# Kernel optimization log

Hardware: AMD Instinct MI355X
Metric: run time of the kernel (lower is better)

Reference implementation:

```python
import jax, jax.numpy as jnp
import numpy as np

N_NODES = 100000
N_EDGES = 1600000
IN_C, HID_C, OUT_C = 128, 128, 64


def gcn_conv(x, src, dst, ew, W, b, n_nodes):
    """PyG GCNConv: symmetric-normalized aggregation with added self-loops.

    out = D^{-1/2} (A + I) D^{-1/2} (x @ W) + b,  D = deg(A+I)
    """
    h = x @ W  # [N, C_out]
    # degree at target nodes, including self-loop weight of 1
    deg = jax.ops.segment_sum(ew, dst, num_segments=n_nodes) + 1.0  # [N]
    dinv = jnp.where(deg > 0, jax.lax.rsqrt(deg), 0.0)
    norm = dinv[src] * ew * dinv[dst]  # [E]
    # gather-scale-scatter over edges + self-loop term (norm_ii = 1/deg_i)
    agg = jax.ops.segment_sum(h[src] * norm[:, None], dst, num_segments=n_nodes)
    agg = agg + h * (dinv * dinv)[:, None]
    return agg + b


def setup_inputs() -> dict:
    key = jax.random.key(0)
    ks = jax.random.split(key, 7)
    x = jax.random.normal(ks[0], (N_NODES, IN_C), dtype=jnp.float32)
    edge_index = jax.random.randint(ks[1], (2, N_EDGES), 0, N_NODES, dtype=jnp.int32)
    edge_weight = jax.random.uniform(ks[2], (N_EDGES,), dtype=jnp.float32)
    W1 = jax.random.normal(ks[3], (IN_C, HID_C), dtype=jnp.float32) / np.sqrt(IN_C)
    b1 = jnp.zeros((HID_C,), dtype=jnp.float32)
    W2 = jax.random.normal(ks[4], (HID_C, OUT_C), dtype=jnp.float32) / np.sqrt(HID_C)
    b2 = jnp.zeros((OUT_C,), dtype=jnp.float32)
    return {"x": x, "edge_index": edge_index, "edge_weight": edge_weight,
            "W1": W1, "b1": b1, "W2": W2, "b2": b2}


def reference(x, edge_index, edge_weight, W1, b1, W2, b2):
    src, dst = edge_index[0], edge_index[1]
    n = x.shape[0]
    h = gcn_conv(x, src, dst, edge_weight, W1, b1, n)
    h = jax.nn.relu(h)
    out = gcn_conv(h, src, dst, edge_weight, W2, b2, n)
    return out
```

## Files before the change

kernel.cpp:

```cpp
#include <hip/hip_runtime.h>


#define N_NODES 100000
#define CHUNK   2048
#define NBUCK   196
#define BSHIFT  9
#define BNODES  512
#define CAP     10240

typedef __attribute__((ext_vector_type(8))) short bf16x8;
typedef __attribute__((ext_vector_type(4))) float f32x4;

__device__ __forceinline__ unsigned bf16r(float f) {
    unsigned u = __float_as_uint(f);
    return (u + 0x7fffu + ((u >> 16) & 1u)) >> 16;
}
__device__ __forceinline__ float bf_lo(unsigned u) { return __uint_as_float(u << 16); }
__device__ __forceinline__ float bf_hi(unsigned u) { return __uint_as_float(u & 0xffff0000u); }

__device__ __forceinline__ void fma8(float* a, uint4 u, float w) {
    a[0] = fmaf(bf_lo(u.x), w, a[0]); a[1] = fmaf(bf_hi(u.x), w, a[1]);
    a[2] = fmaf(bf_lo(u.y), w, a[2]); a[3] = fmaf(bf_hi(u.y), w, a[3]);
    a[4] = fmaf(bf_lo(u.z), w, a[4]); a[5] = fmaf(bf_hi(u.z), w, a[5]);
    a[6] = fmaf(bf_lo(u.w), w, a[6]); a[7] = fmaf(bf_hi(u.w), w, a[7]);
}


__global__ __launch_bounds__(256) void prepA1_kernel(
    const int* __restrict__ dst, const float* __restrict__ W1,
    const float* __restrict__ W2, unsigned* __restrict__ Wt1,
    unsigned* __restrict__ Wt2, int* __restrict__ histmat, int E)
{
    __shared__ int hist[256];
    int t = threadIdx.x;
    if (blockIdx.x == 0) {
        for (int f = t; f < 128 * 64; f += 256) {
            int c = f % 128, j = f / 128;
            Wt1[c * 64 + j] = bf16r(W1[(size_t)(2 * j) * 128 + c]) |
                              (bf16r(W1[(size_t)(2 * j + 1) * 128 + c]) << 16);
        }
        return;
    }
    if (blockIdx.x == 1) {
        for (int f = t; f < 64 * 64; f += 256) {
            int c = f % 64, j = f / 64;
            Wt2[c * 64 + j] = bf16r(W2[(size_t)(2 * j) * 64 + c]) |
                              (bf16r(W2[(size_t)(2 * j + 1) * 64 + c]) << 16);
        }
        return;
    }
    int blk = blockIdx.x - 2;
    hist[t] = 0;
    __syncthreads();
    int e0 = blk * CHUNK;
    int nv = min(CHUNK, E - e0);
#pragma unroll
    for (int j = 0; j < CHUNK / 256; ++j) {
        int idx = t + j * 256;
        if (idx < nv) atomicAdd(&hist[dst[e0 + idx] >> BSHIFT], 1);
    }
    __syncthreads();
    histmat[blk * 256 + t] = hist[t];
}


__global__ __launch_bounds__(256) void scanB_kernel(
    int* __restrict__ histmat, int* __restrict__ bucketSize, int NBLK)
{
    __shared__ int sums[256];
    int b = blockIdx.x, t = threadIdx.x;
    const int PER = (NBLK + 255) / 256;
    int loc[8];
    int s = 0;
#pragma unroll 8
    for (int j = 0; j < PER; ++j) {
        int r = t * PER + j;
        int v = (r < NBLK) ? histmat[r * 256 + b] : 0;
        loc[j] = v; s += v;
    }
    sums[t] = s;
    __syncthreads();
    int v = s;
#pragma unroll
    for (int off = 1; off < 256; off <<= 1) {
        int a = (t >= off) ? sums[t - off] : 0;
        __syncthreads();
        sums[t] += a;
        __syncthreads();
    }
    if (t == 255) bucketSize[b] = sums[255];
    int run = sums[t] - v;
#pragma unroll 8
    for (int j = 0; j < PER; ++j) {
        int r = t * PER + j;
        if (r < NBLK) { histmat[r * 256 + b] = run; run += loc[j]; }
    }
}


__global__ __launch_bounds__(256) void a2_kernel(
    const int* __restrict__ src, const int* __restrict__ dst,
    const float* __restrict__ ew, const int* __restrict__ histmat,
    uint2* __restrict__ csrTmp, int E)
{
    __shared__ int hist[256], sc[256], exc[256], lcur[256], basel[256];
    __shared__ uint2 ent[CHUNK];
    __shared__ unsigned short bof[CHUNK];

    int t = threadIdx.x, blk = blockIdx.x;
    hist[t] = 0; lcur[t] = 0;
    basel[t] = histmat[blk * 256 + t];
    __syncthreads();

    int e0 = blk * CHUNK;
    int nv = min(CHUNK, E - e0);
    int dv[CHUNK / 256]; int sv[CHUNK / 256]; unsigned wv[CHUNK / 256];
#pragma unroll
    for (int j = 0; j < CHUNK / 256; ++j) {
        int idx = t + j * 256;
        if (idx < nv) {
            int e = e0 + idx;
            dv[j] = dst[e]; sv[j] = src[e]; wv[j] = __float_as_uint(ew[e]);
            atomicAdd(&hist[dv[j] >> BSHIFT], 1);
        } else dv[j] = -1;
    }
    __syncthreads();
    int hv = hist[t];
    sc[t] = hv;
    __syncthreads();
#pragma unroll
    for (int off = 1; off < 256; off <<= 1) {
        int a = (t >= off) ? sc[t - off] : 0;
        __syncthreads();
        sc[t] += a;
        __syncthreads();
    }
    exc[t] = sc[t] - hv;
    __syncthreads();
#pragma unroll
    for (int j = 0; j < CHUNK / 256; ++j) {
        if (dv[j] >= 0) {
            int b  = dv[j] >> BSHIFT;
            int dl = dv[j] & (BNODES - 1);
            int p  = exc[b] + atomicAdd(&lcur[b], 1);
            ent[p] = make_uint2(((unsigned)dl << 17) | (unsigned)sv[j], wv[j]);
            bof[p] = (unsigned short)b;
        }
    }
    __syncthreads();
#pragma unroll
    for (int j = 0; j < CHUNK / 256; ++j) {
        int i = t + j * 256;
        if (i < nv) {
            int b = bof[i];
            csrTmp[(size_t)b * CAP + basel[b] + (i - exc[b])] = ent[i];
        }
    }
}


__global__ __launch_bounds__(1024) void bucketB_kernel(
    const uint2* __restrict__ csrTmp, const int* __restrict__ bucketSize,
    float* __restrict__ dinv, uint2* __restrict__ nodeinfo,
    uint2* __restrict__ csrF, int N)
{
    __shared__ uint2 ent[CAP];
    __shared__ unsigned long long dc[BNODES];
    __shared__ int scn[BNODES], beg[BNODES], cur[BNODES];
    int b = blockIdx.x, t = threadIdx.x;
    if (t < BNODES) { dc[t] = 0ull; cur[t] = 0; }
    __syncthreads();

    int sz = min(bucketSize[b], CAP);
    const uint2* reg = csrTmp + (size_t)b * CAP;
    for (int i = t; i < sz; i += 1024) {
        uint2 en = reg[i];
        ent[i] = en;
        int dl = (int)(en.x >> 17);
        unsigned fx = (unsigned)__float2uint_rn(__uint_as_float(en.y) * 16777216.0f);
        atomicAdd(&dc[dl], (1ull << 32) | (unsigned long long)fx);
    }
    __syncthreads();

    int cnt = 0; float dv = 1.0f;
    if (t < BNODES) {
        unsigned long long v = dc[t];
        cnt = (int)(v >> 32);
        dv = rsqrtf((float)(unsigned)(v & 0xffffffffull) * (1.0f / 16777216.0f) + 1.0f);
        scn[t] = cnt;
    }
    __syncthreads();
#pragma unroll
    for (int off = 1; off < BNODES; off <<= 1) {
        int a = 0;
        if (t < BNODES && t >= off) a = scn[t - off];
        __syncthreads();
        if (t < BNODES) scn[t] += a;
        __syncthreads();
    }
    if (t < BNODES) {
        int excl = scn[t] - cnt;
        beg[t] = excl;
        int gn = b * BNODES + t;
        if (gn < N) {
            dinv[gn] = dv;
            nodeinfo[gn] = make_uint2((unsigned)(b * CAP + excl), (unsigned)cnt);
        }
    }
    __syncthreads();

    uint2* outreg = csrF + (size_t)b * CAP;
    for (int i = t; i < sz; i += 1024) {
        uint2 en = ent[i];
        int dl = (int)(en.x >> 17);
        int p  = beg[dl] + atomicAdd(&cur[dl], 1);
        outreg[p] = make_uint2(en.x & 0x1FFFFu, en.y);
    }
}


__global__ __launch_bounds__(256) void gemm1_kernel(
    const float* __restrict__ Xf, const unsigned* __restrict__ Wt,
    const float* __restrict__ dinv, unsigned* __restrict__ Hb, int M)
{
    constexpr int LW = 68, KU = 64;
    __shared__ unsigned sA[64 * LW];
    __shared__ unsigned sB[128 * LW];
    __shared__ float sD[64];
    const int t = threadIdx.x;
    const int rbase = blockIdx.x * 64;

    if (t < 64) sD[t] = (rbase + t < M) ? dinv[rbase + t] : 0.f;
    for (int f = t; f < 128 * 16; f += 256) {
        int c = f >> 4, qd = f & 15;
        *(uint4*)&sB[c * LW + qd * 4] = *(const uint4*)&Wt[c * KU + qd * 4];
    }
    for (int f = t; f < 64 * 32; f += 256) {
        int r = f >> 5, c4 = f & 31;
        int gr = rbase + r;
        float4 v = make_float4(0.f, 0.f, 0.f, 0.f);
        if (gr < M) v = *(const float4*)&Xf[(size_t)gr * 128 + c4 * 4];
        sA[r * LW + c4 * 2]     = bf16r(v.x) | (bf16r(v.y) << 16);
        sA[r * LW + c4 * 2 + 1] = bf16r(v.z) | (bf16r(v.w) << 16);
    }
    __syncthreads();

    const int wave = t >> 6, lane = t & 63;
    const int quad = lane >> 4, lr = lane & 15;
    const int n0 = wave * 32;

    f32x4 acc[4][2];
#pragma unroll
    for (int mi = 0; mi < 4; ++mi)
#pragma unroll
        for (int ni = 0; ni < 2; ++ni)
            acc[mi][ni] = (f32x4){0.f, 0.f, 0.f, 0.f};

#pragma unroll
    for (int ks = 0; ks < 4; ++ks) {
        int ko = ks * 16 + quad * 4;
        bf16x8 b0 = *(const bf16x8*)&sB[(n0 + lr) * LW + ko];
        bf16x8 b1 = *(const bf16x8*)&sB[(n0 + 16 + lr) * LW + ko];
#pragma unroll
        for (int mi = 0; mi < 4; ++mi) {
            bf16x8 a = *(const bf16x8*)&sA[(mi * 16 + lr) * LW + ko];
            acc[mi][0] = __builtin_amdgcn_mfma_f32_16x16x32_bf16(a, b0, acc[mi][0], 0, 0, 0);
            acc[mi][1] = __builtin_amdgcn_mfma_f32_16x16x32_bf16(a, b1, acc[mi][1], 0, 0, 0);
        }
    }
    __syncthreads();

    unsigned short* sO = (unsigned short*)sA;
#pragma unroll
    for (int mi = 0; mi < 4; ++mi)
#pragma unroll
        for (int ni = 0; ni < 2; ++ni)
#pragma unroll
            for (int r = 0; r < 4; ++r) {
                int row = mi * 16 + quad * 4 + r;
                sO[row * (2 * LW) + n0 + ni * 16 + lr] =
                    (unsigned short)bf16r(acc[mi][ni][r] * sD[row]);
            }
    __syncthreads();

    for (int f = t; f < 64 * 64; f += 256) {
        int row = f >> 6, cu = f & 63;
        int gr = rbase + row;
        if (gr < M) Hb[(size_t)gr * 64 + cu] = sA[row * LW + cu];
    }
}


__global__ __launch_bounds__(512, 4) void gg_kernel(
    const uint2* __restrict__ nodeinfo, const uint2* __restrict__ csr,
    const uint4* __restrict__ Hb4,
    const float* __restrict__ dinv, const float* __restrict__ bias,
    const unsigned* __restrict__ Wt2, unsigned* __restrict__ H2, int N)
{
    __shared__ __align__(16) unsigned sG[16 * 68];
    __shared__ __align__(16) float    sO[16 * 68];
    __shared__ float sDi[16];

    const int t = threadIdx.x, wave = t >> 6, lane = t & 63;
    const int q = lane >> 4, cg = lane & 15;
    const int nb = blockIdx.x * 16;
    if (t < 16) sDi[t] = dinv[nb + t];

    const int m0 = wave * 2, m1 = m0 + 1;
    const int n0 = nb + m0, n1 = nb + m1;

    float one0 = (q == 0) ? 1.f : 0.f;
    float acc0[8], acc1[8];
    {
        uint4 su = Hb4[(size_t)n0 * 16 + cg];
        uint4 sv = Hb4[(size_t)n1 * 16 + cg];
        acc0[0] = bf_lo(su.x) * one0; acc0[1] = bf_hi(su.x) * one0;
        acc0[2] = bf_lo(su.y) * one0; acc0[3] = bf_hi(su.y) * one0;
        acc0[4] = bf_lo(su.z) * one0; acc0[5] = bf_hi(su.z) * one0;
        acc0[6] = bf_lo(su.w) * one0; acc0[7] = bf_hi(su.w) * one0;
        acc1[0] = bf_lo(sv.x) * one0; acc1[1] = bf_hi(sv.x) * one0;
        acc1[2] = bf_lo(sv.y) * one0; acc1[3] = bf_hi(sv.y) * one0;
        acc1[4] = bf_lo(sv.z) * one0; acc1[5] = bf_hi(sv.z) * one0;
        acc1[6] = bf_lo(sv.w) * one0; acc1[7] = bf_hi(sv.w) * one0;
    }
    uint2 i0 = nodeinfo[n0], i1 = nodeinfo[n1];
    int j0 = (int)i0.x, e0v = j0 + (int)i0.y;
    int j1 = (int)i1.x, e1v = j1 + (int)i1.y;

    while (j0 < e0v || j1 < e1v) {
        int cs0 = 0, cs1 = 0; float cw0 = 0.f, cw1 = 0.f;
        if (j0 + lane < e0v) { uint2 p = csr[j0 + lane]; cs0 = (int)p.x; cw0 = __uint_as_float(p.y); }
        if (j1 + lane < e1v) { uint2 p = csr[j1 + lane]; cs1 = (int)p.x; cw1 = __uint_as_float(p.y); }
        int r0 = e0v - j0; int mm0 = r0 < 0 ? 0 : (r0 > 64 ? 64 : r0);
        int r1 = e1v - j1; int mm1 = r1 < 0 ? 0 : (r1 > 64 ? 64 : r1);
        int mmx = mm0 > mm1 ? mm0 : mm1;

        int   s0 = __shfl(cs0, q),  s1 = __shfl(cs1, q);
        float w0 = __shfl(cw0, q),  w1 = __shfl(cw1, q);
        uint4 u0 = Hb4[(size_t)s0 * 16 + cg];
        uint4 u1 = Hb4[(size_t)s1 * 16 + cg];

        for (int k = 0; k < mmx; k += 4) {
            uint4 u0n = u0, u1n = u1;
            float w0n = 0.f, w1n = 0.f;
            if (k + 4 < mmx) {
                int s0n = __shfl(cs0, k + 4 + q), s1n = __shfl(cs1, k + 4 + q);
                w0n = __shfl(cw0, k + 4 + q);     w1n = __shfl(cw1, k + 4 + q);
                u0n = Hb4[(size_t)s0n * 16 + cg];
                u1n = Hb4[(size_t)s1n * 16 + cg];
            }
            fma8(acc0, u0, w0);
            fma8(acc1, u1, w1);
            u0 = u0n; u1 = u1n; w0 = w0n; w1 = w1n;
        }
        j0 += 64; j1 += 64;
    }

#pragma unroll
    for (int v = 0; v < 8; ++v) {
        acc0[v] += __shfl_xor(acc0[v], 16);
        acc0[v] += __shfl_xor(acc0[v], 32);
        acc1[v] += __shfl_xor(acc1[v], 16);
        acc1[v] += __shfl_xor(acc1[v], 32);
    }
    if (q == 0) {
        int c = cg * 8;
        float di0 = dinv[n0];
        uint4 pk;
        pk.x = bf16r(fmaxf(acc0[0] * di0 + bias[c + 0], 0.f)) |
               (bf16r(fmaxf(acc0[1] * di0 + bias[c + 1], 0.f)) << 16);
        pk.y = bf16r(fmaxf(acc0[2] * di0 + bias[c + 2], 0.f)) |
               (bf16r(fmaxf(acc0[3] * di0 + bias[c + 3], 0.f)) << 16);
        pk.z = bf16r(fmaxf(acc0[4] * di0 + bias[c + 4], 0.f)) |
               (bf16r(fmaxf(acc0[5] * di0 + bias[c + 5], 0.f)) << 16);
        pk.w = bf16r(fmaxf(acc0[6] * di0 + bias[c + 6], 0.f)) |
               (bf16r(fmaxf(acc0[7] * di0 + bias[c + 7], 0.f)) << 16);
        *(uint4*)&sG[m0 * 68 + cg * 4] = pk;
        float di1 = dinv[n1];
        pk.x = bf16r(fmaxf(acc1[0] * di1 + bias[c + 0], 0.f)) |
               (bf16r(fmaxf(acc1[1] * di1 + bias[c + 1], 0.f)) << 16);
        pk.y = bf16r(fmaxf(acc1[2] * di1 + bias[c + 2], 0.f)) |
               (bf16r(fmaxf(acc1[3] * di1 + bias[c + 3], 0.f)) << 16);
        pk.z = bf16r(fmaxf(acc1[4] * di1 + bias[c + 4], 0.f)) |
               (bf16r(fmaxf(acc1[5] * di1 + bias[c + 5], 0.f)) << 16);
        pk.w = bf16r(fmaxf(acc1[6] * di1 + bias[c + 6], 0.f)) |
               (bf16r(fmaxf(acc1[7] * di1 + bias[c + 7], 0.f)) << 16);
        *(uint4*)&sG[m1 * 68 + cg * 4] = pk;
    }
    __syncthreads();

    if (wave < 4) {
        const int quad = lane >> 4, lr = lane & 15;
        const int nt0 = wave * 16;
        f32x4 accv = (f32x4){0.f, 0.f, 0.f, 0.f};
#pragma unroll
        for (int ks = 0; ks < 4; ++ks) {
            int ko = ks * 16 + quad * 4;
            bf16x8 av = *(const bf16x8*)&sG[lr * 68 + ko];
            bf16x8 bv = *(const bf16x8*)&Wt2[(nt0 + lr) * 64 + ko];
            accv = __builtin_amdgcn_mfma_f32_16x16x32_bf16(av, bv, accv, 0, 0, 0);
        }
#pragma unroll
        for (int r = 0; r < 4; ++r)
            sO[(quad * 4 + r) * 68 + nt0 + lr] = accv[r];
    }
    __syncthreads();

    if (t < 512) {
        int row = t >> 5, cu = t & 31;
        float sc = sDi[row];
        unsigned pk = bf16r(sO[row * 68 + 2 * cu] * sc) |
                      (bf16r(sO[row * 68 + 2 * cu + 1] * sc) << 16);
        H2[(size_t)(nb + row) * 32 + cu] = pk;
    }
}


__global__ __launch_bounds__(256, 4) void gather64_kernel(
    const uint2* __restrict__ nodeinfo, const uint2* __restrict__ csr,
    const uint4* __restrict__ Hb4,
    const float* __restrict__ dinv, const float* __restrict__ bias,
    float* __restrict__ OUT, int N)
{
    const int wave = threadIdx.x >> 6, lane = threadIdx.x & 63;
    const int n0 = blockIdx.x * 8 + wave * 2, n1 = n0 + 1;
    if (n0 >= N) return;
    const int q  = lane >> 3;
    const int cg = lane & 7;

    float one0 = (q == 0) ? 1.f : 0.f;
    float acc0[8], acc1[8];
    {
        uint4 su = Hb4[(size_t)n0 * 8 + cg];
        uint4 sv = Hb4[(size_t)n1 * 8 + cg];
        acc0[0] = bf_lo(su.x) * one0; acc0[1] = bf_hi(su.x) * one0;
        acc0[2] = bf_lo(su.y) * one0; acc0[3] = bf_hi(su.y) * one0;
        acc0[4] = bf_lo(su.z) * one0; acc0[5] = bf_hi(su.z) * one0;
        acc0[6] = bf_lo(su.w) * one0; acc0[7] = bf_hi(su.w) * one0;
        acc1[0] = bf_lo(sv.x) * one0; acc1[1] = bf_hi(sv.x) * one0;
        acc1[2] = bf_lo(sv.y) * one0; acc1[3] = bf_hi(sv.y) * one0;
        acc1[4] = bf_lo(sv.z) * one0; acc1[5] = bf_hi(sv.z) * one0;
        acc1[6] = bf_lo(sv.w) * one0; acc1[7] = bf_hi(sv.w) * one0;
    }

    uint2 i0 = nodeinfo[n0], i1 = nodeinfo[n1];
    int j0 = (int)i0.x, e0v = j0 + (int)i0.y;
    int j1 = (int)i1.x, e1v = j1 + (int)i1.y;

    while (j0 < e0v || j1 < e1v) {
        int cs0 = 0, cs1 = 0; float cw0 = 0.f, cw1 = 0.f;
        if (j0 + lane < e0v) { uint2 p = csr[j0 + lane]; cs0 = (int)p.x; cw0 = __uint_as_float(p.y); }
        if (j1 + lane < e1v) { uint2 p = csr[j1 + lane]; cs1 = (int)p.x; cw1 = __uint_as_float(p.y); }
        int r0 = e0v - j0; int mm0 = r0 < 0 ? 0 : (r0 > 64 ? 64 : r0);
        int r1 = e1v - j1; int mm1 = r1 < 0 ? 0 : (r1 > 64 ? 64 : r1);
        int mmx = mm0 > mm1 ? mm0 : mm1;

        int   s0 = __shfl(cs0, q),  s1 = __shfl(cs1, q);
        float w0 = __shfl(cw0, q),  w1 = __shfl(cw1, q);
        uint4 u0 = Hb4[(size_t)s0 * 8 + cg];
        uint4 u1 = Hb4[(size_t)s1 * 8 + cg];

        for (int k = 0; k < mmx; k += 8) {
            uint4 u0n = u0, u1n = u1;
            float w0n = 0.f, w1n = 0.f;
            if (k + 8 < mmx) {
                int s0n = __shfl(cs0, k + 8 + q), s1n = __shfl(cs1, k + 8 + q);
                w0n = __shfl(cw0, k + 8 + q);     w1n = __shfl(cw1, k + 8 + q);
                u0n = Hb4[(size_t)s0n * 8 + cg];
                u1n = Hb4[(size_t)s1n * 8 + cg];
            }
            fma8(acc0, u0, w0);
            fma8(acc1, u1, w1);
            u0 = u0n; u1 = u1n; w0 = w0n; w1 = w1n;
        }
        j0 += 64; j1 += 64;
    }

#pragma unroll
    for (int v = 0; v < 8; ++v) {
        acc0[v] += __shfl_xor(acc0[v], 8);
        acc0[v] += __shfl_xor(acc0[v], 16);
        acc0[v] += __shfl_xor(acc0[v], 32);
        acc1[v] += __shfl_xor(acc1[v], 8);
        acc1[v] += __shfl_xor(acc1[v], 16);
        acc1[v] += __shfl_xor(acc1[v], 32);
    }

    int c = cg * 8 + q;
    OUT[(size_t)n0 * 64 + c] = acc0[q] * dinv[n0] + bias[c];
    OUT[(size_t)n1 * 64 + c] = acc1[q] * dinv[n1] + bias[c];
}

static inline size_t align_up(size_t x) { return (x + 255) & ~size_t(255); }

extern "C" void kernel_launch(void* const* d_in, const int* in_sizes, int n_in,
                              void* d_out, int out_size, void* d_ws, size_t ws_size,
                              hipStream_t stream)
{
    const float* x  = (const float*)d_in[0];
    const int*   ei = (const int*)d_in[1];
    const float* ew = (const float*)d_in[2];
    const float* W1 = (const float*)d_in[3];
    const float* b1 = (const float*)d_in[4];
    const float* W2 = (const float*)d_in[5];
    const float* b2 = (const float*)d_in[6];
    float* out = (float*)d_out;

    const int N = N_NODES;
    const int E = in_sizes[2];
    const int* src = ei;
    const int* dst = ei + E;

    const int NBLK = (E + CHUNK - 1) / CHUNK;
    const size_t REGION = (size_t)NBUCK * CAP;

    char* ws = (char*)d_ws;
    int*   histmat   = (int*)ws;   ws += align_up((size_t)NBLK * 256 * 4);
    int*   bucketSize= (int*)ws;   ws += align_up((size_t)NBUCK * 4);
    float* dinv      = (float*)ws; ws += align_up((size_t)N * 4);
    uint2* nodeinfo  = (uint2*)ws; ws += align_up((size_t)N * 8);
    uint2* csrTmp    = (uint2*)ws; ws += align_up(REGION * 8);
    uint2* csrF      = (uint2*)ws; ws += align_up(REGION * 8);
    unsigned* Wt1    = (unsigned*)ws; ws += align_up((size_t)128 * 64 * 4);
    unsigned* Wt2    = (unsigned*)ws; ws += align_up((size_t)64 * 64 * 4);
    unsigned* h1     = (unsigned*)ws; ws += align_up((size_t)N * 64 * 4);
    unsigned* h2     = (unsigned*)ws; ws += align_up((size_t)N * 32 * 4);

    prepA1_kernel<<<NBLK + 2, 256, 0, stream>>>(dst, W1, W2, Wt1, Wt2, histmat, E);
    scanB_kernel<<<NBUCK, 256, 0, stream>>>(histmat, bucketSize, NBLK);
    a2_kernel<<<NBLK, 256, 0, stream>>>(src, dst, ew, histmat, csrTmp, E);
    bucketB_kernel<<<NBUCK, 1024, 0, stream>>>(csrTmp, bucketSize, dinv, nodeinfo, csrF, N);
    gemm1_kernel<<<(N + 63) / 64, 256, 0, stream>>>(x, Wt1, dinv, h1, N);
    gg_kernel<<<N / 16, 512, 0, stream>>>(nodeinfo, csrF, (const uint4*)h1,
                                          dinv, b1, Wt2, h2, N);
    gather64_kernel<<<(N + 7) / 8, 256, 0, stream>>>(
        nodeinfo, csrF, (const uint4*)h2, dinv, b2, out, N);
}
```

Measured before the change: 272.6 us.

## Replace two-pass bucketed CSR build with global atomic count-then-scatter

Replaces the histogram/scan/bucket-partition/local-sort pipeline with a simpler build. Per-node 64-bit atomics on global memory accumulate degree count and fixed-point weight sum. A per-bucket scan then computes node offsets, and a scatter kernel places each edge with a global atomic cursor. This removes the csrTmp intermediate pass and two kernels, at the cost of many contended global atomics and random uncoalesced writes. Edge order within a node becomes nondeterministic.

Result: slower. 387.2 us (+42.0%).

```diff
diff --git a/kernel.cpp b/kernel.cpp
--- a/kernel.cpp
+++ b/kernel.cpp
@@ -2,7 +2,6 @@
 
 
 #define N_NODES 100000
-#define CHUNK   2048
 #define NBUCK   196
 #define BSHIFT  9
 #define BNODES  512
@@ -26,12 +25,12 @@
 }
 
 
-__global__ __launch_bounds__(256) void prepA1_kernel(
-    const int* __restrict__ dst, const float* __restrict__ W1,
-    const float* __restrict__ W2, unsigned* __restrict__ Wt1,
-    unsigned* __restrict__ Wt2, int* __restrict__ histmat, int E)
-{
-    __shared__ int hist[256];
+__global__ __launch_bounds__(256) void prepcnt_kernel(
+    const int* __restrict__ dst, const float* __restrict__ ew,
+    const float* __restrict__ W1, const float* __restrict__ W2,
+    unsigned* __restrict__ Wt1, unsigned* __restrict__ Wt2,
+    unsigned long long* __restrict__ degfx, int E)
+{
     int t = threadIdx.x;
     if (blockIdx.x == 0) {
         for (int f = t; f < 128 * 64; f += 256) {
@@ -49,172 +48,62 @@
         }
         return;
     }
-    int blk = blockIdx.x - 2;
-    hist[t] = 0;
-    __syncthreads();
-    int e0 = blk * CHUNK;
-    int nv = min(CHUNK, E - e0);
-#pragma unroll
-    for (int j = 0; j < CHUNK / 256; ++j) {
-        int idx = t + j * 256;
-        if (idx < nv) atomicAdd(&hist[dst[e0 + idx] >> BSHIFT], 1);
-    }
-    __syncthreads();
-    histmat[blk * 256 + t] = hist[t];
-}
-
-
-__global__ __launch_bounds__(256) void scanB_kernel(
-    int* __restrict__ histmat, int* __restrict__ bucketSize, int NBLK)
-{
-    __shared__ int sums[256];
+    int e0 = (blockIdx.x - 2) * 2048;
+#pragma unroll
+    for (int j = 0; j < 8; ++j) {
+        int idx = e0 + t + j * 256;
+        if (idx < E) {
+            unsigned fx = (unsigned)__float2uint_rn(ew[idx] * 16777216.0f);
+            atomicAdd(&degfx[dst[idx]], (1ull << 32) | (unsigned long long)fx);
+        }
+    }
+}
+
+
+__global__ __launch_bounds__(512) void scanN_kernel(
+    const unsigned long long* __restrict__ degfx, float* __restrict__ dinv,
+    uint2* __restrict__ nodeinfo, int* __restrict__ cur, int N)
+{
+    __shared__ int scn[BNODES];
     int b = blockIdx.x, t = threadIdx.x;
-    const int PER = (NBLK + 255) / 256;
-    int loc[8];
-    int s = 0;
-#pragma unroll 8
-    for (int j = 0; j < PER; ++j) {
-        int r = t * PER + j;
-        int v = (r < NBLK) ? histmat[r * 256 + b] : 0;
-        loc[j] = v; s += v;
-    }
-    sums[t] = s;
-    __syncthreads();
-    int v = s;
-#pragma unroll
-    for (int off = 1; off < 256; off <<= 1) {
-        int a = (t >= off) ? sums[t - off] : 0;
+    int gn = b * BNODES + t;
+    unsigned long long v = (gn < N) ? degfx[gn] : 0ull;
+    int cnt = (int)(v >> 32);
+    float dv = rsqrtf((float)(unsigned)(v & 0xffffffffull) * (1.0f / 16777216.0f) + 1.0f);
+    scn[t] = cnt;
+    __syncthreads();
+#pragma unroll
+    for (int off = 1; off < BNODES; off <<= 1) {
+        int a = (t >= off) ? scn[t - off] : 0;
         __syncthreads();
-        sums[t] += a;
+        scn[t] += a;
         __syncthreads();
     }
-    if (t == 255) bucketSize[b] = sums[255];
-    int run = sums[t] - v;
-#pragma unroll 8
-    for (int j = 0; j < PER; ++j) {
-        int r = t * PER + j;
-        if (r < NBLK) { histmat[r * 256 + b] = run; run += loc[j]; }
-    }
-}
-
-
-__global__ __launch_bounds__(256) void a2_kernel(
+    int excl = scn[t] - cnt;
+    if (gn < N) {
+        dinv[gn] = dv;
+        nodeinfo[gn] = make_uint2((unsigned)(b * CAP + excl), (unsigned)cnt);
+        cur[gn] = 0;
+    }
+}
+
+
+__global__ __launch_bounds__(256) void scatter_kernel(
     const int* __restrict__ src, const int* __restrict__ dst,
-    const float* __restrict__ ew, const int* __restrict__ histmat,
-    uint2* __restrict__ csrTmp, int E)
-{
-    __shared__ int hist[256], sc[256], exc[256], lcur[256], basel[256];
-    __shared__ uint2 ent[CHUNK];
-    __shared__ unsigned short bof[CHUNK];
-
-    int t = threadIdx.x, blk = blockIdx.x;
-    hist[t] = 0; lcur[t] = 0;
-    basel[t] = histmat[blk * 256 + t];
-    __syncthreads();
-
-    int e0 = blk * CHUNK;
-    int nv = min(CHUNK, E - e0);
-    int dv[CHUNK / 256]; int sv[CHUNK / 256]; unsigned wv[CHUNK / 256];
-#pragma unroll
-    for (int j = 0; j < CHUNK / 256; ++j) {
-        int idx = t + j * 256;
-        if (idx < nv) {
-            int e = e0 + idx;
-            dv[j] = dst[e]; sv[j] = src[e]; wv[j] = __float_as_uint(ew[e]);
-            atomicAdd(&hist[dv[j] >> BSHIFT], 1);
-        } else dv[j] = -1;
-    }
-    __syncthreads();
-    int hv = hist[t];
-    sc[t] = hv;
-    __syncthreads();
-#pragma unroll
-    for (int off = 1; off < 256; off <<= 1) {
-        int a = (t >= off) ? sc[t - off] : 0;
-        __syncthreads();
-        sc[t] += a;
-        __syncthreads();
-    }
-    exc[t] = sc[t] - hv;
-    __syncthreads();
-#pragma unroll
-    for (int j = 0; j < CHUNK / 256; ++j) {
-        if (dv[j] >= 0) {
-            int b  = dv[j] >> BSHIFT;
-            int dl = dv[j] & (BNODES - 1);
-            int p  = exc[b] + atomicAdd(&lcur[b], 1);
-            ent[p] = make_uint2(((unsigned)dl << 17) | (unsigned)sv[j], wv[j]);
-            bof[p] = (unsigned short)b;
-        }
-    }
-    __syncthreads();
-#pragma unroll
-    for (int j = 0; j < CHUNK / 256; ++j) {
-        int i = t + j * 256;
-        if (i < nv) {
-            int b = bof[i];
-            csrTmp[(size_t)b * CAP + basel[b] + (i - exc[b])] = ent[i];
-        }
-    }
-}
-
-
-__global__ __launch_bounds__(1024) void bucketB_kernel(
-    const uint2* __restrict__ csrTmp, const int* __restrict__ bucketSize,
-    float* __restrict__ dinv, uint2* __restrict__ nodeinfo,
-    uint2* __restrict__ csrF, int N)
-{
-    __shared__ uint2 ent[CAP];
-    __shared__ unsigned long long dc[BNODES];
-    __shared__ int scn[BNODES], beg[BNODES], cur[BNODES];
-    int b = blockIdx.x, t = threadIdx.x;
-    if (t < BNODES) { dc[t] = 0ull; cur[t] = 0; }
-    __syncthreads();
-
-    int sz = min(bucketSize[b], CAP);
-    const uint2* reg = csrTmp + (size_t)b * CAP;
-    for (int i = t; i < sz; i += 1024) {
-        uint2 en = reg[i];
-        ent[i] = en;
-        int dl = (int)(en.x >> 17);
-        unsigned fx = (unsigned)__float2uint_rn(__uint_as_float(en.y) * 16777216.0f);
-        atomicAdd(&dc[dl], (1ull << 32) | (unsigned long long)fx);
-    }
-    __syncthreads();
-
-    int cnt = 0; float dv = 1.0f;
-    if (t < BNODES) {
-        unsigned long long v = dc[t];
-        cnt = (int)(v >> 32);
-        dv = rsqrtf((float)(unsigned)(v & 0xffffffffull) * (1.0f / 16777216.0f) + 1.0f);
-        scn[t] = cnt;
-    }
-    __syncthreads();
-#pragma unroll
-    for (int off = 1; off < BNODES; off <<= 1) {
-        int a = 0;
-        if (t < BNODES && t >= off) a = scn[t - off];
-        __syncthreads();
-        if (t < BNODES) scn[t] += a;
-        __syncthreads();
-    }
-    if (t < BNODES) {
-        int excl = scn[t] - cnt;
-        beg[t] = excl;
-        int gn = b * BNODES + t;
-        if (gn < N) {
-            dinv[gn] = dv;
-            nodeinfo[gn] = make_uint2((unsigned)(b * CAP + excl), (unsigned)cnt);
-        }
-    }
-    __syncthreads();
-
-    uint2* outreg = csrF + (size_t)b * CAP;
-    for (int i = t; i < sz; i += 1024) {
-        uint2 en = ent[i];
-        int dl = (int)(en.x >> 17);
-        int p  = beg[dl] + atomicAdd(&cur[dl], 1);
-        outreg[p] = make_uint2(en.x & 0x1FFFFu, en.y);
+    const float* __restrict__ ew, const unsigned* __restrict__ nodebase,
+    int* __restrict__ cur, uint2* __restrict__ csrF, int E)
+{
+    int e0 = blockIdx.x * 2048;
+    int t = threadIdx.x;
+#pragma unroll
+    for (int j = 0; j < 8; ++j) {
+        int idx = e0 + t + j * 256;
+        if (idx < E) {
+            int d = dst[idx];
+            unsigned base = nodebase[(size_t)d * 2];
+            int p = atomicAdd(&cur[d], 1);
+            csrF[base + p] = make_uint2((unsigned)src[idx], __float_as_uint(ew[idx]));
+        }
     }
 }
 
@@ -511,26 +400,26 @@
     const int* src = ei;
     const int* dst = ei + E;
 
-    const int NBLK = (E + CHUNK - 1) / CHUNK;
     const size_t REGION = (size_t)NBUCK * CAP;
+    const int EBLK = (E + 2047) / 2048;
 
     char* ws = (char*)d_ws;
-    int*   histmat   = (int*)ws;   ws += align_up((size_t)NBLK * 256 * 4);
-    int*   bucketSize= (int*)ws;   ws += align_up((size_t)NBUCK * 4);
+    unsigned long long* degfx = (unsigned long long*)ws; ws += align_up((size_t)N * 8);
+    int*   cur       = (int*)ws;   ws += align_up((size_t)N * 4);
     float* dinv      = (float*)ws; ws += align_up((size_t)N * 4);
     uint2* nodeinfo  = (uint2*)ws; ws += align_up((size_t)N * 8);
-    uint2* csrTmp    = (uint2*)ws; ws += align_up(REGION * 8);
     uint2* csrF      = (uint2*)ws; ws += align_up(REGION * 8);
     unsigned* Wt1    = (unsigned*)ws; ws += align_up((size_t)128 * 64 * 4);
     unsigned* Wt2    = (unsigned*)ws; ws += align_up((size_t)64 * 64 * 4);
     unsigned* h1     = (unsigned*)ws; ws += align_up((size_t)N * 64 * 4);
     unsigned* h2     = (unsigned*)ws; ws += align_up((size_t)N * 32 * 4);
 
-    prepA1_kernel<<<NBLK + 2, 256, 0, stream>>>(dst, W1, W2, Wt1, Wt2, histmat, E);
-    scanB_kernel<<<NBUCK, 256, 0, stream>>>(histmat, bucketSize, NBLK);
-    a2_kernel<<<NBLK, 256, 0, stream>>>(src, dst, ew, histmat, csrTmp, E);
-    bucketB_kernel<<<NBUCK, 1024, 0, stream>>>(csrTmp, bucketSize, dinv, nodeinfo, csrF, N);
+    hipMemsetAsync(degfx, 0, (size_t)N * 8, stream);
+    prepcnt_kernel<<<EBLK + 2, 256, 0, stream>>>(dst, ew, W1, W2, Wt1, Wt2, degfx, E);
+    scanN_kernel<<<NBUCK, 512, 0, stream>>>(degfx, dinv, nodeinfo, cur, N);
     gemm1_kernel<<<(N + 63) / 64, 256, 0, stream>>>(x, Wt1, dinv, h1, N);
+    scatter_kernel<<<EBLK, 256, 0, stream>>>(src, dst, ew, (const unsigned*)nodeinfo,
+                                             cur, csrF, E);
     gg_kernel<<<N / 16, 512, 0, stream>>>(nodeinfo, csrF, (const uint4*)h1,
                                           dinv, b1, Wt2, h2, N);
     gather64_kernel<<<(N + 7) / 8, 256, 0, stream>>>(
```

## Replace histogram/scan/scatter passes with atomic bucket reservation in one kernel

Applied to the files above, without the earlier changes.

Merges the per-chunk histogram kernel, the global column scan kernel and the scatter kernel into a single kernel. Each block now reserves its slice of every destination bucket with a global atomicAdd on a bucket cursor instead of reading precomputed scan offsets. This removes two kernel launches and a full extra read of the dst array and histmat. The cost is a memset and nondeterministic ordering of edges within buckets, which can change floating-point summation order and locality.

Result: no change. 272.5 us (median of 2 runs) (-0.1%).

```diff
diff --git a/kernel.cpp b/kernel.cpp
--- a/kernel.cpp
+++ b/kernel.cpp
@@ -26,12 +26,17 @@
 }
 
 
-__global__ __launch_bounds__(256) void prepA1_kernel(
-    const int* __restrict__ dst, const float* __restrict__ W1,
+__global__ __launch_bounds__(256) void a2F_kernel(
+    const int* __restrict__ src, const int* __restrict__ dst,
+    const float* __restrict__ ew, const float* __restrict__ W1,
     const float* __restrict__ W2, unsigned* __restrict__ Wt1,
-    unsigned* __restrict__ Wt2, int* __restrict__ histmat, int E)
-{
-    __shared__ int hist[256];
+    unsigned* __restrict__ Wt2, int* __restrict__ bucketCur,
+    uint2* __restrict__ csrTmp, int E)
+{
+    __shared__ int hist[256], sc[256], exc[256], lcur[256], basel[256];
+    __shared__ uint2 ent[CHUNK];
+    __shared__ unsigned short bof[CHUNK];
+
     int t = threadIdx.x;
     if (blockIdx.x == 0) {
         for (int f = t; f < 128 * 64; f += 256) {
@@ -50,66 +55,7 @@
         return;
     }
     int blk = blockIdx.x - 2;
-    hist[t] = 0;
-    __syncthreads();
-    int e0 = blk * CHUNK;
-    int nv = min(CHUNK, E - e0);
-#pragma unroll
-    for (int j = 0; j < CHUNK / 256; ++j) {
-        int idx = t + j * 256;
-        if (idx < nv) atomicAdd(&hist[dst[e0 + idx] >> BSHIFT], 1);
-    }
-    __syncthreads();
-    histmat[blk * 256 + t] = hist[t];
-}
-
-
-__global__ __launch_bounds__(256) void scanB_kernel(
-    int* __restrict__ histmat, int* __restrict__ bucketSize, int NBLK)
-{
-    __shared__ int sums[256];
-    int b = blockIdx.x, t = threadIdx.x;
-    const int PER = (NBLK + 255) / 256;
-    int loc[8];
-    int s = 0;
-#pragma unroll 8
-    for (int j = 0; j < PER; ++j) {
-        int r = t * PER + j;
-        int v = (r < NBLK) ? histmat[r * 256 + b] : 0;
-        loc[j] = v; s += v;
-    }
-    sums[t] = s;
-    __syncthreads();
-    int v = s;
-#pragma unroll
-    for (int off = 1; off < 256; off <<= 1) {
-        int a = (t >= off) ? sums[t - off] : 0;
-        __syncthreads();
-        sums[t] += a;
-        __syncthreads();
-    }
-    if (t == 255) bucketSize[b] = sums[255];
-    int run = sums[t] - v;
-#pragma unroll 8
-    for (int j = 0; j < PER; ++j) {
-        int r = t * PER + j;
-        if (r < NBLK) { histmat[r * 256 + b] = run; run += loc[j]; }
-    }
-}
-
-
-__global__ __launch_bounds__(256) void a2_kernel(
-    const int* __restrict__ src, const int* __restrict__ dst,
-    const float* __restrict__ ew, const int* __restrict__ histmat,
-    uint2* __restrict__ csrTmp, int E)
-{
-    __shared__ int hist[256], sc[256], exc[256], lcur[256], basel[256];
-    __shared__ uint2 ent[CHUNK];
-    __shared__ unsigned short bof[CHUNK];
-
-    int t = threadIdx.x, blk = blockIdx.x;
     hist[t] = 0; lcur[t] = 0;
-    basel[t] = histmat[blk * 256 + t];
     __syncthreads();
 
     int e0 = blk * CHUNK;
@@ -136,6 +82,7 @@
         __syncthreads();
     }
     exc[t] = sc[t] - hv;
+    basel[t] = (hv > 0) ? atomicAdd(&bucketCur[t], hv) : 0;
     __syncthreads();
 #pragma unroll
     for (int j = 0; j < CHUNK / 256; ++j) {
@@ -515,8 +462,7 @@
     const size_t REGION = (size_t)NBUCK * CAP;
 
     char* ws = (char*)d_ws;
-    int*   histmat   = (int*)ws;   ws += align_up((size_t)NBLK * 256 * 4);
-    int*   bucketSize= (int*)ws;   ws += align_up((size_t)NBUCK * 4);
+    int*   bucketCur = (int*)ws;   ws += align_up((size_t)NBUCK * 4);
     float* dinv      = (float*)ws; ws += align_up((size_t)N * 4);
     uint2* nodeinfo  = (uint2*)ws; ws += align_up((size_t)N * 8);
     uint2* csrTmp    = (uint2*)ws; ws += align_up(REGION * 8);
@@ -526,10 +472,10 @@
     unsigned* h1     = (unsigned*)ws; ws += align_up((size_t)N * 64 * 4);
     unsigned* h2     = (unsigned*)ws; ws += align_up((size_t)N * 32 * 4);
 
-    prepA1_kernel<<<NBLK + 2, 256, 0, stream>>>(dst, W1, W2, Wt1, Wt2, histmat, E);
-    scanB_kernel<<<NBUCK, 256, 0, stream>>>(histmat, bucketSize, NBLK);
-    a2_kernel<<<NBLK, 256, 0, stream>>>(src, dst, ew, histmat, csrTmp, E);
-    bucketB_kernel<<<NBUCK, 1024, 0, stream>>>(csrTmp, bucketSize, dinv, nodeinfo, csrF, N);
+    hipMemsetAsync(bucketCur, 0, (size_t)NBUCK * 4, stream);
+    a2F_kernel<<<NBLK + 2, 256, 0, stream>>>(src, dst, ew, W1, W2,
+                                             Wt1, Wt2, bucketCur, csrTmp, E);
+    bucketB_kernel<<<NBUCK, 1024, 0, stream>>>(csrTmp, bucketCur, dinv, nodeinfo, csrF, N);
     gemm1_kernel<<<(N + 63) / 64, 256, 0, stream>>>(x, Wt1, dinv, h1, N);
     gg_kernel<<<N / 16, 512, 0, stream>>>(nodeinfo, csrF, (const uint4*)h1,
                                           dinv, b1, Wt2, h2, N);
```
